# Kernel optimization log

Hardware: AMD Instinct MI355X
Metric: run time of the kernel (lower is better)

## Reference

```python
import jax, jax.numpy as jnp
import numpy as np

B, H, W, C = 8, 64, 64, 256  # N = H*W = 4096, pooled length N//2 = 2048


def setup_inputs() -> dict:
    key = jax.random.key(0)
    k1, k2, k3, k4 = jax.random.split(key, 4)
    scale = np.sqrt(2.0 / C).astype(np.float32)  # he_normal for 1x1 conv
    return {
        "x": jax.random.normal(k1, (B, H, W, C), dtype=jnp.float32),
        "w_theta": jax.random.normal(k2, (C, C), dtype=jnp.float32) * scale,
        "w_phi": jax.random.normal(k3, (C, C), dtype=jnp.float32) * scale,
        "w_g": jax.random.normal(k4, (C, C), dtype=jnp.float32) * scale,
    }


def _maxpool1d(z):
    # MaxPool1D(pool_size=2, strides=2, padding='valid') over axis 1
    b, n, c = z.shape
    return jnp.max(z.reshape(b, n // 2, 2, c), axis=2)


def reference(x, w_theta, w_phi, w_g):
    b, h, w, c = x.shape
    n = h * w
    xf = x.reshape(b, n, c)                       # [B, N, C]
    theta = xf @ w_theta                          # [B, N, C] (1x1 conv)
    phi = _maxpool1d(xf @ w_phi)                  # [B, N//2, C]
    f = jnp.einsum('bnc,bmc->bnm', theta, phi)    # [B, N, N//2] affinity
    f = jax.nn.softmax(f, axis=-1)
    g = _maxpool1d(xf @ w_g)                      # [B, N//2, C]
    y = jnp.einsum('bnm,bmc->bnc', f, g)          # [B, N, C]
    y = y.reshape(b, h, w, c)
    return x + y                                  # residual
```

## Files before the change

kernel.cpp:

```cpp
#include <hip/hip_runtime.h>
#include <stdint.h>

#define CC 256
#define NN 4096
#define MM 2048
#define BB 8
#define NROWS (BB*NN)
#define PROWS (BB*MM)

typedef __attribute__((ext_vector_type(8))) short    short8;
typedef __attribute__((ext_vector_type(8))) _Float16 half8;
typedef __attribute__((ext_vector_type(4))) float    float4v;

__device__ __forceinline__ unsigned short f2bf(float f) {
    unsigned int u = __float_as_uint(f);
    u += 0x7fffu + ((u >> 16) & 1u);
    return (unsigned short)(u >> 16);
}
__device__ __forceinline__ float bf2f(unsigned short h) {
    return __uint_as_float(((unsigned int)h) << 16);
}
__device__ __forceinline__ unsigned short f2h(float f) {
    union { _Float16 h; unsigned short u; } cv; cv.h = (_Float16)f; return cv.u;
}
__device__ __forceinline__ float h2f(unsigned short u) {
    union { _Float16 h; unsigned short u; } cv; cv.u = u; return (float)cv.h;
}

__global__ __launch_bounds__(256) void xsplit_kernel(
    const float* __restrict__ x,
    unsigned short* __restrict__ x_hi,
    unsigned short* __restrict__ x_lo)
{
    const size_t i = ((size_t)blockIdx.x*256 + threadIdx.x) * 8;
    float4v a0 = *(const float4v*)(x + i);
    float4v a1 = *(const float4v*)(x + i + 4);
    short8 h, l;
    #pragma unroll
    for (int j = 0; j < 4; ++j) {
        unsigned short h0 = f2bf(a0[j]);
        h[j]   = (short)h0; l[j]   = (short)f2bf(a0[j] - bf2f(h0));
        unsigned short h1 = f2bf(a1[j]);
        h[4+j] = (short)h1; l[4+j] = (short)f2bf(a1[j] - bf2f(h1));
    }
    *(short8*)(x_hi + i) = h;
    *(short8*)(x_lo + i) = l;
}

__global__ void wsplit_kernel(const float* __restrict__ w_theta,
                              const float* __restrict__ w_phi,
                              const float* __restrict__ w_g,
                              unsigned short* __restrict__ wT_hi,
                              unsigned short* __restrict__ wT_lo)
{
    __shared__ float tile[64][65];
    const int widx = blockIdx.z;
    const int kt = blockIdx.x, ct = blockIdx.y;
    const float* w = (widx == 0) ? w_theta : (widx == 1) ? w_phi : w_g;
    const int t  = threadIdx.x;
    const int tc = t & 63, tr = t >> 6;
    #pragma unroll
    for (int i = 0; i < 16; ++i) {
        const int lk = tr*16 + i;
        tile[lk][tc] = w[(size_t)(kt*64 + lk)*CC + ct*64 + tc];
    }
    __syncthreads();
    #pragma unroll
    for (int i = 0; i < 16; ++i) {
        const int lc = tr*16 + i;
        float v = tile[tc][lc];
        const int c = ct*64 + lc, k = kt*64 + tc;
        unsigned short hh = f2bf(v);
        size_t o = ((size_t)widx*CC + c)*CC + k;
        wT_hi[o] = hh;
        wT_lo[o] = f2bf(v - bf2f(hh));
    }
}

__global__ __launch_bounds__(256, 4) void proj_kernel(
    const unsigned short* __restrict__ x_hi,
    const unsigned short* __restrict__ x_lo,
    const unsigned short* __restrict__ wT_hi,
    const unsigned short* __restrict__ wT_lo,
    unsigned short* __restrict__ th,
    unsigned short* __restrict__ ph,
    unsigned short* __restrict__ g_f)
{
    __shared__ unsigned short wt_hi[64*136];
    __shared__ unsigned short wt_lo[64*136];

    const int tid  = threadIdx.x;
    const int rb   = blockIdx.x & 511;
    const int cv   = blockIdx.x >> 9;
    const int r0   = rb * 64;
    const int widx = cv >> 2;
    const int wc0  = (cv & 3) * 64;
    const unsigned short* wThp = wT_hi + ((size_t)widx*CC + wc0)*CC;
    const unsigned short* wTlp = wT_lo + ((size_t)widx*CC + wc0)*CC;
    const bool split3 = (widx < 2);

    const int wv   = tid >> 6;
    const int lane = tid & 63;
    const int quad = lane >> 4;
    const int l15  = lane & 15;
    const int arow = r0 + wv*16 + l15;
    const unsigned short* axh = x_hi + (size_t)arow*CC + quad*8;
    const unsigned short* axl = x_lo + (size_t)arow*CC + quad*8;

    float4v acc[4];
    #pragma unroll
    for (int nf = 0; nf < 4; ++nf) acc[nf] = (float4v){0.f,0.f,0.f,0.f};

    for (int h = 0; h < 2; ++h) {
        __syncthreads();
        {
            const int j    = tid & 63;
            const int kseg = tid >> 6;
            const size_t base = (size_t)j*CC + h*128 + kseg*32;
            const unsigned short* sh = wThp + base;
            unsigned short* dh = &wt_hi[j*136 + kseg*32];
            #pragma unroll
            for (int u = 0; u < 4; ++u)
                *(uint4*)(dh + u*8) = *(const uint4*)(sh + u*8);
            if (split3) {
                const unsigned short* sl = wTlp + base;
                unsigned short* dl = &wt_lo[j*136 + kseg*32];
                #pragma unroll
                for (int u = 0; u < 4; ++u)
                    *(uint4*)(dl + u*8) = *(const uint4*)(sl + u*8);
            }
        }
        __syncthreads();

        #pragma unroll
        for (int ks = 0; ks < 4; ++ks) {
            short8 a_hi = *(const short8*)(axh + h*128 + ks*32);
            short8 a_lo;
            if (split3) a_lo = *(const short8*)(axl + h*128 + ks*32);
            #pragma unroll
            for (int nf = 0; nf < 4; ++nf) {
                const int wrow = nf*16 + l15;
                short8 b_hi = *(const short8*)&wt_hi[wrow*136 + ks*32 + quad*8];
                acc[nf] = __builtin_amdgcn_mfma_f32_16x16x32_bf16(a_hi, b_hi, acc[nf], 0,0,0);
                if (split3) {
                    short8 b_lo = *(const short8*)&wt_lo[wrow*136 + ks*32 + quad*8];
                    acc[nf] = __builtin_amdgcn_mfma_f32_16x16x32_bf16(a_hi, b_lo, acc[nf], 0,0,0);
                    acc[nf] = __builtin_amdgcn_mfma_f32_16x16x32_bf16(a_lo, b_hi, acc[nf], 0,0,0);
                }
            }
        }
    }

    const int rowbase = r0 + wv*16 + quad*4;
    if (widx == 0) {
        #pragma unroll
        for (int nf = 0; nf < 4; ++nf) {
            const int c = wc0 + nf*16 + l15;
            #pragma unroll
            for (int r = 0; r < 4; ++r)
                th[(size_t)(rowbase + r)*CC + c] = f2h(acc[nf][r]);
        }
    } else if (widx == 1) {
        #pragma unroll
        for (int nf = 0; nf < 4; ++nf) {
            const int c = wc0 + nf*16 + l15;
            #pragma unroll
            for (int rp = 0; rp < 2; ++rp) {
                float v = fmaxf(acc[nf][2*rp], acc[nf][2*rp+1]);
                const int prow = rowbase/2 + rp;
                ph[(size_t)prow*CC + c] = f2h(v);
            }
        }
    } else {
        #pragma unroll
        for (int nf = 0; nf < 4; ++nf) {
            const int c = wc0 + nf*16 + l15;
            const int ct = c >> 4;
            const int c15 = c & 15;
            #pragma unroll
            for (int rp = 0; rp < 2; ++rp) {
                float v = fmaxf(acc[nf][2*rp], acc[nf][2*rp+1]);
                const int prow = rowbase/2 + rp;
                const int b  = prow >> 11;
                const int m  = prow & 2047;
                const int kt = m >> 5;
                const int km = m & 31;
                const int lane_t = (km >> 3)*16 + c15;
                const int j = km & 7;
                g_f[(((size_t)(b*64 + kt)*16 + ct)*64 + lane_t)*8 + j] = f2bf(v);
            }
        }
    }
}

__global__ void phimean_kernel(const unsigned short* __restrict__ ph,
                               float* __restrict__ phbar)
{
    const int b = blockIdx.x >> 6, chunk = blockIdx.x & 63;
    const int c = threadIdx.x;
    const size_t base = ((size_t)b*MM + chunk*32)*CC + c;
    float s = 0.f;
    for (int r = 0; r < 32; ++r) s += h2f(ph[base + (size_t)r*CC]);
    atomicAdd(&phbar[b*CC + c], s * (1.0f/MM));
}

__global__ __launch_bounds__(256, 3) void attn_kernel(
    const float* __restrict__ x,
    const unsigned short* __restrict__ th,
    const unsigned short* __restrict__ ph,
    const unsigned short* __restrict__ g_f,
    const float* __restrict__ phbar,
    float* __restrict__ out)
{
    __shared__ unsigned short s_ph[2][32*264];
    __shared__ unsigned short s_p[4][16*40];
    __shared__ float          s_l[64];

    const int tid  = threadIdx.x;
    const int bb   = blockIdx.x & 7;
    const int qt   = blockIdx.x >> 3;
    const int q0   = bb*NN + qt*64;
    const int b    = bb;
    const int wv   = tid >> 6;
    const int lane = tid & 63;
    const int quad = lane >> 4;
    const int l15  = lane & 15;

    const size_t phbase = (size_t)b * MM * CC;
    const unsigned short* stsrc = ph + phbase + (size_t)tid*8;
    const int ldsbase = (tid >> 5)*264 + (tid & 31)*8;

    half8 t_hi[8];
    {
        const unsigned short* bh = th + (size_t)(q0 + wv*16 + l15)*CC;
        #pragma unroll
        for (int ks = 0; ks < 8; ++ks)
            t_hi[ks] = *(const half8*)(bh + ks*32 + quad*8);
    }

    float sh128[4];
    {
        float sp = 0.f;
        #pragma unroll
        for (int ks = 0; ks < 8; ++ks) {
            const int k0 = ks*32 + quad*8;
            float4v m0 = *(const float4v*)&phbar[b*CC + k0];
            float4v m1 = *(const float4v*)&phbar[b*CC + k0 + 4];
            #pragma unroll
            for (int j = 0; j < 4; ++j) {
                sp += (float)t_hi[ks][j]   * m0[j];
                sp += (float)t_hi[ks][4+j] * m1[j];
            }
        }
        sp += __shfl_xor(sp, 16);
        sp += __shfl_xor(sp, 32);
        #pragma unroll
        for (int r = 0; r < 4; ++r)
            sh128[r] = __shfl(sp, quad*4 + r) + 128.f;
    }

    float4v O[4][4];
    #pragma unroll
    for (int rt = 0; rt < 4; ++rt)
        #pragma unroll
        for (int ct = 0; ct < 4; ++ct) O[rt][ct] = (float4v){0.f,0.f,0.f,0.f};
    float4v accl = (float4v){0.f,0.f,0.f,0.f};

    short8 ones;
    #pragma unroll
    for (int j = 0; j < 8; ++j) ones[j] = (short)0x3F80;

    const unsigned short* glf = g_f + (size_t)b*MM*CC + (size_t)lane*8;

    {
        #pragma unroll
        for (int u = 0; u < 4; ++u)
            *(uint4*)(&s_ph[0][ldsbase + u*2112]) =
                *(const uint4*)(stsrc + u*2048);
    }
    __syncthreads();

    for (int kt = 0; kt < 64; ++kt) {
        const int key0 = kt * 32;  (void)key0;
        const int cur  = kt & 1;

        uint4 stg[4];
        if (kt < 63) {
            const unsigned short* sn = stsrc + (size_t)(kt + 1)*8192;
            #pragma unroll
            for (int u = 0; u < 4; ++u)
                stg[u] = *(const uint4*)(sn + u*2048);
        }
        short8 gf[4];
        #pragma unroll
        for (int ct = 0; ct < 4; ++ct)
            gf[ct] = *(const short8*)(glf + (size_t)(kt*16 + wv*4 + ct)*512);

        float4v S0 = (float4v){0.f,0.f,0.f,0.f};
        float4v S1 = (float4v){0.f,0.f,0.f,0.f};
        #pragma unroll
        for (int ks = 0; ks < 8; ++ks) {
            half8 b0 = *(const half8*)&s_ph[cur][( 0 + l15)*264 + ks*32 + quad*8];
            half8 b1 = *(const half8*)&s_ph[cur][(16 + l15)*264 + ks*32 + quad*8];
            S0 = __builtin_amdgcn_mfma_f32_16x16x32_f16(t_hi[ks], b0, S0, 0,0,0);
            S1 = __builtin_amdgcn_mfma_f32_16x16x32_f16(t_hi[ks], b1, S1, 0,0,0);
        }

        unsigned short* pw = &s_p[wv][0];
        #pragma unroll
        for (int r = 0; r < 4; ++r) {
            float a0 = fminf(fmaxf(S0[r] - sh128[r], -85.f), 85.f);
            float a1 = fminf(fmaxf(S1[r] - sh128[r], -85.f), 85.f);
            pw[(quad*4 + r)*40 + l15]      = f2bf(__expf(a0));
            pw[(quad*4 + r)*40 + 16 + l15] = f2bf(__expf(a1));
        }
        asm volatile("s_waitcnt lgkmcnt(0)" ::: "memory");
        short8 pown = *(const short8*)&s_p[wv][l15*40 + quad*8];
        accl = __builtin_amdgcn_mfma_f32_16x16x32_bf16(pown, ones, accl, 0,0,0);

        if (kt < 63) {
            #pragma unroll
            for (int u = 0; u < 4; ++u)
                *(uint4*)(&s_ph[cur ^ 1][ldsbase + u*2112]) = stg[u];
        }
        __syncthreads();

        #pragma unroll
        for (int rt = 0; rt < 4; ++rt) {
            short8 pA = *(const short8*)&s_p[rt][l15*40 + quad*8];
            #pragma unroll
            for (int ct = 0; ct < 4; ++ct)
                O[rt][ct] = __builtin_amdgcn_mfma_f32_16x16x32_bf16(pA, gf[ct], O[rt][ct], 0,0,0);
        }
        __syncthreads();
    }

    if (l15 == 0) {
        #pragma unroll
        for (int r = 0; r < 4; ++r) s_l[wv*16 + quad*4 + r] = accl[r];
    }
    __syncthreads();

    #pragma unroll
    for (int rt = 0; rt < 4; ++rt) {
        #pragma unroll
        for (int r = 0; r < 4; ++r) {
            const int row = q0 + rt*16 + quad*4 + r;
            const float rl = 1.0f / s_l[rt*16 + quad*4 + r];
            #pragma unroll
            for (int ct = 0; ct < 4; ++ct) {
                const int c = wv*64 + ct*16 + l15;
                const size_t idx = (size_t)row*CC + c;
                out[idx] = x[idx] + O[rt][ct][r] * rl;
            }
        }
    }
}

extern "C" void kernel_launch(void* const* d_in, const int* in_sizes, int n_in,
                              void* d_out, int out_size, void* d_ws, size_t ws_size,
                              hipStream_t stream) {
    const float* x       = (const float*)d_in[0];
    const float* w_theta = (const float*)d_in[1];
    const float* w_phi   = (const float*)d_in[2];
    const float* w_g     = (const float*)d_in[3];
    float* out = (float*)d_out;

    unsigned short* th    = (unsigned short*)d_ws;
    unsigned short* ph    = th    + (size_t)NROWS*CC;
    unsigned short* g_f   = ph    + (size_t)PROWS*CC;
    unsigned short* x_hi  = g_f   + (size_t)PROWS*CC;
    unsigned short* x_lo  = x_hi  + (size_t)NROWS*CC;
    unsigned short* wT_hi = x_lo  + (size_t)NROWS*CC;
    unsigned short* wT_lo = wT_hi + (size_t)3*CC*CC;
    float*          phbar = (float*)(wT_lo + (size_t)3*CC*CC);

    hipMemsetAsync(phbar, 0, BB*CC*sizeof(float), stream);
    xsplit_kernel<<<NROWS*CC/8/256, 256, 0, stream>>>(x, x_hi, x_lo);
    wsplit_kernel<<<dim3(4,4,3), 256, 0, stream>>>(w_theta, w_phi, w_g, wT_hi, wT_lo);
    proj_kernel<<<6144, 256, 0, stream>>>(x_hi, x_lo, wT_hi, wT_lo, th, ph, g_f);
    phimean_kernel<<<512, 256, 0, stream>>>(ph, phbar);
    attn_kernel<<<NROWS/64, 256, 0, stream>>>(x, th, ph, g_f, phbar, out);
}
```

Before: 265.0 us.

## Keep softmax probabilities in registers via transposed MFMA and lane shuffles

The QK^T MFMA operands are swapped so each lane holds transposed scores, and the exponentiated probabilities are packed to bf16 and redistributed with lane shuffles into the A-operand layout. This removes the per-tile LDS round trip for P, the second block barrier, and the ones-vector MFMA used for row sums. Each wave now owns its 16 query rows across all 256 output channels, so it holds 16 accumulator tiles and loads 16 g fragments per step. Register pressure roughly doubles, and launch bounds drop from 3 to 2 blocks per SIMD, which reduces occupancy.

```diff
diff --git a/kernel.cpp b/kernel.cpp
--- a/kernel.cpp
+++ b/kernel.cpp
@@ -204,7 +204,7 @@
     atomicAdd(&phbar[b*CC + c], s * (1.0f/MM));
 }
 
-__global__ __launch_bounds__(256, 3) void attn_kernel(
+__global__ __launch_bounds__(256, 2) void attn_kernel(
     const float* __restrict__ x,
     const unsigned short* __restrict__ th,
     const unsigned short* __restrict__ ph,
@@ -213,8 +213,6 @@
     float* __restrict__ out)
 {
     __shared__ unsigned short s_ph[2][32*264];
-    __shared__ unsigned short s_p[4][16*40];
-    __shared__ float          s_l[64];
 
     const int tid  = threadIdx.x;
     const int bb   = blockIdx.x & 7;
@@ -238,7 +236,7 @@
             t_hi[ks] = *(const half8*)(bh + ks*32 + quad*8);
     }
 
-    float sh128[4];
+    float sh;
     {
         float sp = 0.f;
         #pragma unroll
@@ -254,21 +252,13 @@
         }
         sp += __shfl_xor(sp, 16);
         sp += __shfl_xor(sp, 32);
-        #pragma unroll
-        for (int r = 0; r < 4; ++r)
-            sh128[r] = __shfl(sp, quad*4 + r) + 128.f;
-    }
-
-    float4v O[4][4];
-    #pragma unroll
-    for (int rt = 0; rt < 4; ++rt)
-        #pragma unroll
-        for (int ct = 0; ct < 4; ++ct) O[rt][ct] = (float4v){0.f,0.f,0.f,0.f};
-    float4v accl = (float4v){0.f,0.f,0.f,0.f};
-
-    short8 ones;
-    #pragma unroll
-    for (int j = 0; j < 8; ++j) ones[j] = (short)0x3F80;
+        sh = sp + 128.f;
+    }
+
+    float4v O[16];
+    #pragma unroll
+    for (int ct = 0; ct < 16; ++ct) O[ct] = (float4v){0.f,0.f,0.f,0.f};
+    float laccum = 0.f;
 
     const unsigned short* glf = g_f + (size_t)b*MM*CC + (size_t)lane*8;
 
@@ -280,9 +270,10 @@
     }
     __syncthreads();
 
+    const int srcb = ((quad & 1) << 5) + l15;
+
     for (int kt = 0; kt < 64; ++kt) {
-        const int key0 = kt * 32;  (void)key0;
-        const int cur  = kt & 1;
+        const int cur = kt & 1;
 
         uint4 stg[4];
         if (kt < 63) {
@@ -291,68 +282,84 @@
             for (int u = 0; u < 4; ++u)
                 stg[u] = *(const uint4*)(sn + u*2048);
         }
-        short8 gf[4];
-        #pragma unroll
-        for (int ct = 0; ct < 4; ++ct)
-            gf[ct] = *(const short8*)(glf + (size_t)(kt*16 + wv*4 + ct)*512);
-
-        float4v S0 = (float4v){0.f,0.f,0.f,0.f};
-        float4v S1 = (float4v){0.f,0.f,0.f,0.f};
+        short8 gf[16];
+        #pragma unroll
+        for (int ct = 0; ct < 16; ++ct)
+            gf[ct] = *(const short8*)(glf + (size_t)(kt*16 + ct)*512);
+
+        float4v S0T = (float4v){0.f,0.f,0.f,0.f};
+        float4v S1T = (float4v){0.f,0.f,0.f,0.f};
         #pragma unroll
         for (int ks = 0; ks < 8; ++ks) {
             half8 b0 = *(const half8*)&s_ph[cur][( 0 + l15)*264 + ks*32 + quad*8];
             half8 b1 = *(const half8*)&s_ph[cur][(16 + l15)*264 + ks*32 + quad*8];
-            S0 = __builtin_amdgcn_mfma_f32_16x16x32_f16(t_hi[ks], b0, S0, 0,0,0);
-            S1 = __builtin_amdgcn_mfma_f32_16x16x32_f16(t_hi[ks], b1, S1, 0,0,0);
-        }
-
-        unsigned short* pw = &s_p[wv][0];
+            S0T = __builtin_amdgcn_mfma_f32_16x16x32_f16(b0, t_hi[ks], S0T, 0,0,0);
+            S1T = __builtin_amdgcn_mfma_f32_16x16x32_f16(b1, t_hi[ks], S1T, 0,0,0);
+        }
+
+        float e0[4], e1[4];
         #pragma unroll
         for (int r = 0; r < 4; ++r) {
-            float a0 = fminf(fmaxf(S0[r] - sh128[r], -85.f), 85.f);
-            float a1 = fminf(fmaxf(S1[r] - sh128[r], -85.f), 85.f);
-            pw[(quad*4 + r)*40 + l15]      = f2bf(__expf(a0));
-            pw[(quad*4 + r)*40 + 16 + l15] = f2bf(__expf(a1));
-        }
-        asm volatile("s_waitcnt lgkmcnt(0)" ::: "memory");
-        short8 pown = *(const short8*)&s_p[wv][l15*40 + quad*8];
-        accl = __builtin_amdgcn_mfma_f32_16x16x32_bf16(pown, ones, accl, 0,0,0);
+            e0[r] = __expf(fminf(fmaxf(S0T[r] - sh, -85.f), 85.f));
+            e1[r] = __expf(fminf(fmaxf(S1T[r] - sh, -85.f), 85.f));
+        }
+        unsigned int c00 = (unsigned int)f2bf(e0[0]) | ((unsigned int)f2bf(e0[1]) << 16);
+        unsigned int c01 = (unsigned int)f2bf(e0[2]) | ((unsigned int)f2bf(e0[3]) << 16);
+        unsigned int c10 = (unsigned int)f2bf(e1[0]) | ((unsigned int)f2bf(e1[1]) << 16);
+        unsigned int c11 = (unsigned int)f2bf(e1[2]) | ((unsigned int)f2bf(e1[3]) << 16);
+
+        unsigned int a00 = (unsigned int)__shfl((int)c00, srcb);
+        unsigned int a01 = (unsigned int)__shfl((int)c01, srcb);
+        unsigned int b00 = (unsigned int)__shfl((int)c00, srcb + 16);
+        unsigned int b01 = (unsigned int)__shfl((int)c01, srcb + 16);
+        unsigned int a10 = (unsigned int)__shfl((int)c10, srcb);
+        unsigned int a11 = (unsigned int)__shfl((int)c11, srcb);
+        unsigned int b10 = (unsigned int)__shfl((int)c10, srcb + 16);
+        unsigned int b11 = (unsigned int)__shfl((int)c11, srcb + 16);
+        const bool sel = (quad < 2);
+        union PU { unsigned int u[4]; short8 s8; } pu;
+        pu.u[0] = sel ? a00 : a10;
+        pu.u[1] = sel ? a01 : a11;
+        pu.u[2] = sel ? b00 : b10;
+        pu.u[3] = sel ? b01 : b11;
+        short8 pa = pu.s8;
+
+        {
+            float s = bf2f((unsigned short)(pu.u[0] & 0xffff)) + bf2f((unsigned short)(pu.u[0] >> 16))
+                    + bf2f((unsigned short)(pu.u[1] & 0xffff)) + bf2f((unsigned short)(pu.u[1] >> 16))
+                    + bf2f((unsigned short)(pu.u[2] & 0xffff)) + bf2f((unsigned short)(pu.u[2] >> 16))
+                    + bf2f((unsigned short)(pu.u[3] & 0xffff)) + bf2f((unsigned short)(pu.u[3] >> 16));
+            laccum += s;
+        }
 
         if (kt < 63) {
             #pragma unroll
             for (int u = 0; u < 4; ++u)
                 *(uint4*)(&s_ph[cur ^ 1][ldsbase + u*2112]) = stg[u];
         }
+
+        #pragma unroll
+        for (int ct = 0; ct < 16; ++ct)
+            O[ct] = __builtin_amdgcn_mfma_f32_16x16x32_bf16(pa, gf[ct], O[ct], 0,0,0);
+
         __syncthreads();
-
-        #pragma unroll
-        for (int rt = 0; rt < 4; ++rt) {
-            short8 pA = *(const short8*)&s_p[rt][l15*40 + quad*8];
-            #pragma unroll
-            for (int ct = 0; ct < 4; ++ct)
-                O[rt][ct] = __builtin_amdgcn_mfma_f32_16x16x32_bf16(pA, gf[ct], O[rt][ct], 0,0,0);
-        }
-        __syncthreads();
-    }
-
-    if (l15 == 0) {
-        #pragma unroll
-        for (int r = 0; r < 4; ++r) s_l[wv*16 + quad*4 + r] = accl[r];
-    }
-    __syncthreads();
-
-    #pragma unroll
-    for (int rt = 0; rt < 4; ++rt) {
+    }
+
+    laccum += __shfl_xor(laccum, 16);
+    laccum += __shfl_xor(laccum, 32);
+    float rl[4];
+    #pragma unroll
+    for (int r = 0; r < 4; ++r)
+        rl[r] = 1.0f / __shfl(laccum, quad*4 + r);
+
+    #pragma unroll
+    for (int ct = 0; ct < 16; ++ct) {
         #pragma unroll
         for (int r = 0; r < 4; ++r) {
-            const int row = q0 + rt*16 + quad*4 + r;
-            const float rl = 1.0f / s_l[rt*16 + quad*4 + r];
-            #pragma unroll
-            for (int ct = 0; ct < 4; ++ct) {
-                const int c = wv*64 + ct*16 + l15;
-                const size_t idx = (size_t)row*CC + c;
-                out[idx] = x[idx] + O[rt][ct][r] * rl;
-            }
+            const int row = q0 + wv*16 + quad*4 + r;
+            const int c   = ct*16 + l15;
+            const size_t idx = (size_t)row*CC + c;
+            out[idx] = x[idx] + O[ct][r] * rl[r];
         }
     }
 }
```

After: 285.9 us. +7.9%, slower.
